# Kernel tuning notes

Measured on AMD Instinct MI355X. Metric: run time of the kernel, lower is better.

Reference implementation:

```python
import jax, jax.numpy as jnp
import numpy as np

D_MODEL = 1024
N_HEADS = 16
HEAD_DIM = D_MODEL // N_HEADS


def setup_inputs() -> dict:
    key = jax.random.key(0)
    k1, k2, k3 = jax.random.split(key, 3)
    B, T, C = 4, 2048, D_MODEL
    x = jax.random.normal(k1, (B, T, C), dtype=jnp.float32)
    # torch Linear weight is (out,in); store as (in,out) so y = x @ W
    w_qkv = jax.random.normal(k2, (C, 3 * C), dtype=jnp.float32) * (1.0 / np.sqrt(C))
    w_proj = jax.random.normal(k3, (C, C), dtype=jnp.float32) * (1.0 / np.sqrt(C))
    return {"x": x, "w_qkv": w_qkv, "w_proj": w_proj}


def reference(x, w_qkv, w_proj):
    B, T, C = x.shape
    H, Dh = N_HEADS, HEAD_DIM
    qkv = x @ w_qkv                        # (B,T,3C)
    q, k, v = jnp.split(qkv, 3, axis=-1)
    def heads(t):
        return t.reshape(B, T, H, Dh).transpose(0, 2, 1, 3)  # (B,H,T,Dh)
    q, k, v = heads(q), heads(k), heads(v)
    scores = jnp.einsum('bhqd,bhkd->bhqk', q, k) / np.sqrt(Dh).astype(np.float32)
    causal = jnp.tril(jnp.ones((T, T), dtype=bool))
    scores = jnp.where(causal, scores, -jnp.inf)
    attn = jax.nn.softmax(scores, axis=-1)
    y = jnp.einsum('bhqk,bhkd->bhqd', attn, v)  # (B,H,T,Dh)
    y = y.transpose(0, 2, 1, 3).reshape(B, T, C)
    return y @ w_proj
```

## Files before the change

### kernel.cpp

```cpp
#include <hip/hip_runtime.h>

#define SEQ_T 2048
#define NBATCH 4
#define CDIM 1024
#define NHEAD 16
#define MROWS 8192
#define QKVC 3072

typedef unsigned short u16;
typedef __bf16 bf16x8 __attribute__((ext_vector_type(8)));
typedef float f32x4 __attribute__((ext_vector_type(4)));
typedef unsigned short u16x8 __attribute__((ext_vector_type(8)));
typedef unsigned uint32x4 __attribute__((ext_vector_type(4)));

__device__ __forceinline__ u16 f32_to_bf16(float f) {
  union { float f; unsigned int u; } v; v.f = f;
  unsigned int u = v.u;
  unsigned int r = ((u >> 16) & 1u) + 0x7fffu;
  return (u16)((u + r) >> 16);
}

__device__ __forceinline__ void gload_lds16(const u16* g, u16* l) {
  __builtin_amdgcn_global_load_lds(
      (const __attribute__((address_space(1))) void*)g,
      (__attribute__((address_space(3))) void*)l, 16, 0, 0);
}

__global__ __launch_bounds__(256) void cast_bf16_kernel(const float* __restrict__ in,
                                                        u16* __restrict__ out, int n4) {
  int i = blockIdx.x * 256 + threadIdx.x;
  if (i >= n4) return;
  float4 v = ((const float4*)in)[i];
  ushort4 o;
  o.x = f32_to_bf16(v.x); o.y = f32_to_bf16(v.y);
  o.z = f32_to_bf16(v.z); o.w = f32_to_bf16(v.w);
  ((ushort4*)out)[i] = o;
}

__global__ void transpose_cast_kernel(const float* __restrict__ in, u16* __restrict__ out,
                                      int R, int Cc) {
  __shared__ float tile[32][33];
  int c0 = blockIdx.x * 32, r0 = blockIdx.y * 32;
  int tx = threadIdx.x, ty = threadIdx.y;
  #pragma unroll
  for (int i = 0; i < 32; i += 8)
    tile[ty + i][tx] = in[(size_t)(r0 + ty + i) * Cc + c0 + tx];
  __syncthreads();
  #pragma unroll
  for (int i = 0; i < 32; i += 8)
    out[(size_t)(c0 + ty + i) * R + r0 + tx] = f32_to_bf16(tile[tx][ty + i]);
}

__global__ __launch_bounds__(256) void repack_k_kernel(const u16* __restrict__ QKV,
                                                       u16* __restrict__ Kc) {
  const int kvt32 = blockIdx.x, bh = blockIdx.y;
  const int b = bh >> 4, h = bh & 15;
  const int tid = threadIdx.x;
  const int f = tid >> 6, l = tid & 63;
  const int t = f >> 1, i = f & 1;
  const int row = kvt32 * 32 + t * 16 + (l & 15);
  const bf16x8 v = *(const bf16x8*)(QKV + (size_t)b * SEQ_T * QKVC + (size_t)row * QKVC +
                                    CDIM + h * 64 + i * 32 + (l >> 4) * 8);
  *(bf16x8*)(Kc + (size_t)bh * 131072 + (size_t)kvt32 * 2048 + f * 512 + l * 8) = v;
}

__global__ void repack_v_kernel(const u16* __restrict__ QKV, u16* __restrict__ Vc) {
  __shared__ u16 tile[32][34];
  const int t0 = blockIdx.x * 32, d0 = blockIdx.y * 32;
  const int bh = blockIdx.z;
  const int b = bh >> 4, h = bh & 15;
  const int tx = threadIdx.x, ty = threadIdx.y;
  const u16* Vp = QKV + (size_t)b * SEQ_T * QKVC + 2 * CDIM + h * 64 + d0;
  #pragma unroll
  for (int i = 0; i < 32; i += 8)
    tile[ty + i][tx] = Vp[(size_t)(t0 + ty + i) * QKVC + tx];
  __syncthreads();
  const int tid = ty * 32 + tx;
  if (tid < 128) {
    const int bc = tid >> 2, ag = tid & 3;
    union { u16 u[8]; bf16x8 v; } o;
    #pragma unroll
    for (int j = 0; j < 8; ++j) o.u[j] = tile[ag * 8 + j][bc];
    const int dvl = d0 + bc;
    *(bf16x8*)(Vc + (size_t)bh * 131072 + (size_t)(t0 >> 5) * 2048 +
               (dvl >> 4) * 512 + ag * 128 + (dvl & 15) * 8) = o.v;
  }
}

template <typename OT, bool QSCALE>
__global__ __launch_bounds__(256, 3)
void gemm_bt_kernel(const u16* __restrict__ A, const u16* __restrict__ Bt,
                    OT* __restrict__ C, int N, int K) {
  __shared__ u16 sA[3][4096];
  __shared__ u16 sB[3][4096];
  const int tid = threadIdx.x;
  const int lane = tid & 63, w = tid >> 6;
  const int wm = w >> 1, wn = w & 1;
  const int l15 = lane & 15, lhi = lane >> 4;
  const int row0 = blockIdx.x * 128, col0 = blockIdx.y * 128;

  const int oln  = ((lane & 3) - (lane >> 2)) & 3;
  const int srow = w * 32 + (lane >> 2);
  const u16* aS = A  + (size_t)(row0 + srow) * K + oln * 8;
  const u16* bS = Bt + (size_t)(col0 + srow) * K + oln * 8;
  const int stD = w * 1024;
  const int rdA = (wm * 64 + l15) * 32 + ((lhi + l15) & 3) * 8;
  const int rdB = (wn * 64 + l15) * 32 + ((lhi + l15) & 3) * 8;

  f32x4 acc[4][4] = {};

#define STAGE(KT, S)                                                            \
  {                                                                             \
    const size_t ko = (size_t)(KT) * 32;                                        \
    gload_lds16(aS + ko,          &sA[S][stD]);                                 \
    gload_lds16(aS + ko + 16 * K, &sA[S][stD + 512]);                           \
    gload_lds16(bS + ko,          &sB[S][stD]);                                 \
    gload_lds16(bS + ko + 16 * K, &sB[S][stD + 512]);                           \
  }
#define COMPUTE(S)                                                              \
  {                                                                             \
    bf16x8 af[4], bf[4];                                                        \
    _Pragma("unroll") for (int mi = 0; mi < 4; ++mi)                            \
      af[mi] = *(const bf16x8*)&sA[S][rdA + mi * 512];                          \
    _Pragma("unroll") for (int ni = 0; ni < 4; ++ni)                            \
      bf[ni] = *(const bf16x8*)&sB[S][rdB + ni * 512];                          \
    __builtin_amdgcn_s_setprio(1);                                              \
    _Pragma("unroll") for (int mi = 0; mi < 4; ++mi)                            \
      _Pragma("unroll") for (int ni = 0; ni < 4; ++ni)                          \
        acc[mi][ni] = __builtin_amdgcn_mfma_f32_16x16x32_bf16(af[mi], bf[ni],   \
                                                              acc[mi][ni], 0, 0, 0); \
    __builtin_amdgcn_s_setprio(0);                                              \
  }
#define WAITBAR4                                                                \
  asm volatile("s_waitcnt vmcnt(4)" ::: "memory");                              \
  __builtin_amdgcn_sched_barrier(0);                                            \
  __builtin_amdgcn_s_barrier();

  STAGE(0, 0);
  STAGE(1, 1);
  WAITBAR4;

  #pragma unroll 1
  for (int kt = 0; kt < 30; kt += 3) {
    STAGE(kt + 2, 2); COMPUTE(0); WAITBAR4;
    STAGE(kt + 3, 0); COMPUTE(1); WAITBAR4;
    STAGE(kt + 4, 1); COMPUTE(2); WAITBAR4;
  }
  COMPUTE(0);
  asm volatile("s_waitcnt vmcnt(0)" ::: "memory");
  __builtin_amdgcn_sched_barrier(0);
  __builtin_amdgcn_s_barrier();
  COMPUTE(1);
#undef STAGE
#undef COMPUTE
#undef WAITBAR4

  #pragma unroll
  for (int mt = 0; mt < 4; ++mt)
    #pragma unroll
    for (int nt = 0; nt < 4; ++nt)
      #pragma unroll
      for (int r = 0; r < 4; ++r) {
        const int rr = row0 + wm * 64 + mt * 16 + lhi * 4 + r;
        const int cc = col0 + wn * 64 + nt * 16 + l15;
        float v = acc[mt][nt][r];
        if (QSCALE && cc < CDIM) v *= 0.18033688011f;
        if constexpr (sizeof(OT) == 2) C[(size_t)rr * N + cc] = f32_to_bf16(v);
        else                           C[(size_t)rr * N + cc] = v;
      }
}

template <bool DOMASK>
__device__ __forceinline__ void attn_step(const bf16x8 (&qf)[2],
                                          const bf16x8 (&kf)[2][2],
                                          const bf16x8 (&vb)[4],
                                          const bf16x8 ones,
                                          f32x4 (&acc)[4], f32x4& acc1,
                                          int l15, int lhi, int kv0, int qg) {
  f32x4 st[2];
  #pragma unroll
  for (int t = 0; t < 2; ++t) {
    f32x4 z = {0.f, 0.f, 0.f, 0.f};
    z = __builtin_amdgcn_mfma_f32_16x16x32_bf16(kf[t][0], qf[0], z, 0, 0, 0);
    z = __builtin_amdgcn_mfma_f32_16x16x32_bf16(kf[t][1], qf[1], z, 0, 0, 0);
    st[t] = z;
  }
  #pragma unroll
  for (int t = 0; t < 2; ++t)
    #pragma unroll
    for (int r = 0; r < 4; ++r) {
      float sv = st[t][r];
      if (DOMASK) {
        const int kvg = kv0 + t * 16 + lhi * 4 + r;
        sv = (kvg > qg) ? -__builtin_inff() : sv;
      }
      st[t][r] = exp2f(sv);
    }
  unsigned c00, c01, c10, c11;
  asm("v_cvt_pk_bf16_f32 %0, %1, %2" : "=v"(c00) : "v"(st[0][0]), "v"(st[0][1]));
  asm("v_cvt_pk_bf16_f32 %0, %1, %2" : "=v"(c01) : "v"(st[0][2]), "v"(st[0][3]));
  asm("v_cvt_pk_bf16_f32 %0, %1, %2" : "=v"(c10) : "v"(st[1][0]), "v"(st[1][1]));
  asm("v_cvt_pk_bf16_f32 %0, %1, %2" : "=v"(c11) : "v"(st[1][2]), "v"(st[1][3]));
  asm("v_permlane32_swap_b32 %0, %1" : "+v"(c00), "+v"(c10));
  asm("v_permlane32_swap_b32 %0, %1" : "+v"(c01), "+v"(c11));
  asm("v_permlane16_swap_b32 %0, %1" : "+v"(c00), "+v"(c10));
  asm("v_permlane16_swap_b32 %0, %1" : "+v"(c01), "+v"(c11));
  uint32x4 pw; pw[0] = c00; pw[1] = c01; pw[2] = c10; pw[3] = c11;
  const bf16x8 pa = __builtin_bit_cast(bf16x8, pw);
  #pragma unroll
  for (int d = 0; d < 4; ++d)
    acc[d] = __builtin_amdgcn_mfma_f32_16x16x32_bf16(pa, vb[d], acc[d], 0, 0, 0);
  acc1 = __builtin_amdgcn_mfma_f32_16x16x32_bf16(pa, ones, acc1, 0, 0, 0);
}

__global__ __launch_bounds__(256, 4) void attn_kernel(const u16* __restrict__ QKV,
                                                      const u16* __restrict__ Kc,
                                                      const u16* __restrict__ Vc,
                                                      u16* __restrict__ Y) {
  __shared__ u16 Kl[2][2048];
  __shared__ u16 Vl[2][2048];
  const int tid = threadIdx.x, lane = tid & 63, wid = tid >> 6;
  const int l15 = lane & 15, lhi = lane >> 4;
  const int id = blockIdx.x;
  const int xcd = id & 7, k = (id >> 3) & 15, hi3 = id >> 7;
  const int bh = hi3 * 8 + xcd;
  const int b = bh >> 4, h = bh & 15;
  const int pa = k * 4 + wid;
  const int qA0 = pa * 16, qB0 = (127 - pa) * 16;
  const int nchA = pa / 2 + 1, nchB = (127 - pa) / 2 + 1;
  const int ncmax = (127 - k * 4) / 2 + 1;
  const size_t base = (size_t)b * SEQ_T * QKVC;
  const u16* Qp  = QKV + base + h * 64;
  const u16* KcC = Kc + (size_t)bh * 131072;
  const u16* VcC = Vc + (size_t)bh * 131072;

  u16x8 ou;
  #pragma unroll
  for (int j = 0; j < 8; ++j) ou[j] = 0x3F80;
  const bf16x8 ones = __builtin_bit_cast(bf16x8, ou);

  gload_lds16(KcC + wid * 512 + lane * 8, &Kl[0][wid * 512]);
  gload_lds16(VcC + wid * 512 + lane * 8, &Vl[0][wid * 512]);

  bf16x8 qfA[2], qfB[2];
  #pragma unroll
  for (int i = 0; i < 2; ++i) {
    qfA[i] = *(const bf16x8*)(Qp + (size_t)(qA0 + l15) * QKVC + i * 32 + lhi * 8);
    qfB[i] = *(const bf16x8*)(Qp + (size_t)(qB0 + l15) * QKVC + i * 32 + lhi * 8);
  }
  const int qgA = qA0 + l15, qgB = qB0 + l15;

  f32x4 accA[4] = {}, accB[4] = {};
  f32x4 acc1A = {}, acc1B = {};

  __syncthreads();

  int cbuf = 0;
  for (int ic = 0; ic < ncmax; ++ic) {
    if (ic + 1 < ncmax) {
      const u16* kg = KcC + (size_t)(ic + 1) * 2048 + wid * 512 + lane * 8;
      const u16* vg = VcC + (size_t)(ic + 1) * 2048 + wid * 512 + lane * 8;
      gload_lds16(kg, &Kl[cbuf ^ 1][wid * 512]);
      gload_lds16(vg, &Vl[cbuf ^ 1][wid * 512]);
    }
    const u16* kb = &Kl[cbuf][0];
    const u16* vp = &Vl[cbuf][0];
    bf16x8 kf[2][2], vb[4];
    #pragma unroll
    for (int t = 0; t < 2; ++t)
      #pragma unroll
      for (int i = 0; i < 2; ++i)
        kf[t][i] = *(const bf16x8*)(kb + (t * 2 + i) * 512 + lane * 8);
    #pragma unroll
    for (int d = 0; d < 4; ++d)
      vb[d] = *(const bf16x8*)(vp + d * 512 + lane * 8);

    const int kv0 = ic * 32;
    if (ic < nchB) {
      if (ic == nchB - 1)
        attn_step<true>(qfB, kf, vb, ones, accB, acc1B, l15, lhi, kv0, qgB);
      else
        attn_step<false>(qfB, kf, vb, ones, accB, acc1B, l15, lhi, kv0, qgB);
    }
    if (ic < nchA) {
      if (ic == nchA - 1)
        attn_step<true>(qfA, kf, vb, ones, accA, acc1A, l15, lhi, kv0, qgA);
      else
        attn_step<false>(qfA, kf, vb, ones, accA, acc1A, l15, lhi, kv0, qgA);
    }
    __syncthreads();
    cbuf ^= 1;
  }

  u16* Yp = Y + (size_t)b * SEQ_T * CDIM + h * 64;
  #pragma unroll
  for (int r = 0; r < 4; ++r) {
    const float ivA = 1.0f / acc1A[r];
    const float ivB = 1.0f / acc1B[r];
    #pragma unroll
    for (int d = 0; d < 4; ++d) {
      Yp[(size_t)(qA0 + lhi * 4 + r) * CDIM + d * 16 + l15] = f32_to_bf16(accA[d][r] * ivA);
      Yp[(size_t)(qB0 + lhi * 4 + r) * CDIM + d * 16 + l15] = f32_to_bf16(accB[d][r] * ivB);
    }
  }
}

extern "C" void kernel_launch(void* const* d_in, const int* in_sizes, int n_in,
                              void* d_out, int out_size, void* d_ws, size_t ws_size,
                              hipStream_t stream) {
  const float* x      = (const float*)d_in[0];
  const float* w_qkv  = (const float*)d_in[1];
  const float* w_proj = (const float*)d_in[2];
  float* out = (float*)d_out;

  u16* Xb  = (u16*)d_ws;
  u16* Wqt = Xb  + (size_t)MROWS * CDIM;
  u16* Wpt = Wqt + (size_t)QKVC * CDIM;
  u16* QKV = Wpt + (size_t)CDIM * CDIM;
  u16* Yb  = QKV + (size_t)MROWS * QKVC;
  u16* Vc  = Yb  + (size_t)MROWS * CDIM;
  u16* Kc  = Xb;

  cast_bf16_kernel<<<(MROWS * CDIM / 4 + 255) / 256, 256, 0, stream>>>(x, Xb, MROWS * CDIM / 4);
  transpose_cast_kernel<<<dim3(QKVC / 32, CDIM / 32), dim3(32, 8), 0, stream>>>(w_qkv, Wqt, CDIM, QKVC);
  transpose_cast_kernel<<<dim3(CDIM / 32, CDIM / 32), dim3(32, 8), 0, stream>>>(w_proj, Wpt, CDIM, CDIM);

  gemm_bt_kernel<u16, true><<<dim3(MROWS / 128, QKVC / 128), 256, 0, stream>>>(Xb, Wqt, QKV, QKVC, CDIM);

  repack_k_kernel<<<dim3(SEQ_T / 32, NBATCH * NHEAD), 256, 0, stream>>>(QKV, Kc);
  repack_v_kernel<<<dim3(SEQ_T / 32, 2, NBATCH * NHEAD), dim3(32, 8), 0, stream>>>(QKV, Vc);

  attn_kernel<<<1024, 256, 0, stream>>>(QKV, Kc, Vc, Yb);

  gemm_bt_kernel<float, false><<<dim3(MROWS / 128, CDIM / 128), 256, 0, stream>>>(Yb, Wpt, out, CDIM, CDIM);
}
```

Baseline: 189.0 us.

## Pre-tile QKV GEMM operands into MFMA fragment layout and use 256x256 tiles

The cast kernels for x and w_qkv now write bf16 data directly in a 16x32 fragment-tiled layout, so each wave fetches a contiguous 1KB fragment. This lets the new GEMM load straight to LDS without swizzling. The QKV projection moves to a new 256x256-tile kernel with 512 threads, triple-buffered LDS and per-wave 128x64 accumulators, which raises arithmetic intensity. In exchange it uses more registers and LDS per block, and the grid shrinks to 384 blocks, which may underfill the 256 CUs.

After: 194.3 us. 2.8% more time.

```diff
diff --git a/kernel.cpp b/kernel.cpp
--- a/kernel.cpp
+++ b/kernel.cpp
@@ -26,15 +26,44 @@
       (__attribute__((address_space(3))) void*)l, 16, 0, 0);
 }
 
-__global__ __launch_bounds__(256) void cast_bf16_kernel(const float* __restrict__ in,
-                                                        u16* __restrict__ out, int n4) {
-  int i = blockIdx.x * 256 + threadIdx.x;
-  if (i >= n4) return;
-  float4 v = ((const float4*)in)[i];
-  ushort4 o;
-  o.x = f32_to_bf16(v.x); o.y = f32_to_bf16(v.y);
-  o.z = f32_to_bf16(v.z); o.w = f32_to_bf16(v.w);
-  ((ushort4*)out)[i] = o;
+
+__global__ __launch_bounds__(256) void cast_block_kernel(const float* __restrict__ in,
+                                                         u16* __restrict__ out) {
+  const int i = blockIdx.x * 256 + threadIdx.x;
+  const int kg = i & 127;
+  const int row = i >> 7;
+  const float4 v0 = ((const float4*)in)[i * 2];
+  const float4 v1 = ((const float4*)in)[i * 2 + 1];
+  union { u16 u[8]; bf16x8 b; } o;
+  o.u[0] = f32_to_bf16(v0.x); o.u[1] = f32_to_bf16(v0.y);
+  o.u[2] = f32_to_bf16(v0.z); o.u[3] = f32_to_bf16(v0.w);
+  o.u[4] = f32_to_bf16(v1.x); o.u[5] = f32_to_bf16(v1.y);
+  o.u[6] = f32_to_bf16(v1.z); o.u[7] = f32_to_bf16(v1.w);
+  const int tile = (row >> 4) * 32 + (kg >> 2);
+  const int lane = (row & 15) + ((kg & 3) << 4);
+  *(bf16x8*)(out + (size_t)tile * 512 + lane * 8) = o.b;
+}
+
+__global__ void transpose_cast_block_kernel(const float* __restrict__ in,
+                                            u16* __restrict__ out) {
+  __shared__ float tile[32][33];
+  const int c0 = blockIdx.x * 32, r0 = blockIdx.y * 32;
+  const int tx = threadIdx.x, ty = threadIdx.y;
+  #pragma unroll
+  for (int i = 0; i < 32; i += 8)
+    tile[ty + i][tx] = in[(size_t)(r0 + ty + i) * QKVC + c0 + tx];
+  __syncthreads();
+  const int t = ty * 32 + tx;
+  if (t < 128) {
+    const int cc = t & 31, kgq = t >> 5;
+    union { u16 u[8]; bf16x8 b; } o;
+    #pragma unroll
+    for (int j = 0; j < 8; ++j) o.u[j] = f32_to_bf16(tile[kgq * 8 + j][cc]);
+    const int rowN = c0 + cc;
+    const int tileI = (rowN >> 4) * 32 + (r0 >> 5);
+    const int lane = (rowN & 15) + (kgq << 4);
+    *(bf16x8*)(out + (size_t)tileI * 512 + lane * 8) = o.b;
+  }
 }
 
 __global__ void transpose_cast_kernel(const float* __restrict__ in, u16* __restrict__ out,
@@ -85,6 +114,84 @@
     *(bf16x8*)(Vc + (size_t)bh * 131072 + (size_t)(t0 >> 5) * 2048 +
                (dvl >> 4) * 512 + ag * 128 + (dvl & 15) * 8) = o.v;
   }
+}
+
+template <bool QSCALE>
+__global__ __launch_bounds__(512, 2)
+void gemm256_kernel(const u16* __restrict__ Ab, const u16* __restrict__ Bb,
+                    u16* __restrict__ C, int N) {
+  __shared__ u16 sA[3][8192];
+  __shared__ u16 sB[3][8192];
+  const int tid = threadIdx.x;
+  const int lane = tid & 63, w = tid >> 6;
+  const int wm = w >> 2, wn = w & 3;
+  const int l15 = lane & 15, lhi = lane >> 4;
+  const int row0 = blockIdx.x * 256, col0 = blockIdx.y * 256;
+
+  const u16* aT0 = Ab + ((size_t)((row0 >> 4) + w)     * 32) * 512 + lane * 8;
+  const u16* aT1 = Ab + ((size_t)((row0 >> 4) + 8 + w) * 32) * 512 + lane * 8;
+  const u16* bT0 = Bb + ((size_t)((col0 >> 4) + w)     * 32) * 512 + lane * 8;
+  const u16* bT1 = Bb + ((size_t)((col0 >> 4) + 8 + w) * 32) * 512 + lane * 8;
+
+  f32x4 acc[8][4] = {};
+
+#define STAGE(KT, S)                                                            \
+  {                                                                             \
+    gload_lds16(aT0 + (size_t)(KT) * 512, &sA[S][w * 512]);                     \
+    gload_lds16(aT1 + (size_t)(KT) * 512, &sA[S][(8 + w) * 512]);               \
+    gload_lds16(bT0 + (size_t)(KT) * 512, &sB[S][w * 512]);                     \
+    gload_lds16(bT1 + (size_t)(KT) * 512, &sB[S][(8 + w) * 512]);               \
+  }
+#define COMPUTE(S)                                                              \
+  {                                                                             \
+    bf16x8 bf[4];                                                               \
+    _Pragma("unroll") for (int ni = 0; ni < 4; ++ni)                            \
+      bf[ni] = *(const bf16x8*)&sB[S][(wn * 4 + ni) * 512 + lane * 8];          \
+    __builtin_amdgcn_s_setprio(1);                                              \
+    _Pragma("unroll") for (int mi = 0; mi < 8; ++mi) {                          \
+      const bf16x8 af = *(const bf16x8*)&sA[S][(wm * 8 + mi) * 512 + lane * 8]; \
+      _Pragma("unroll") for (int ni = 0; ni < 4; ++ni)                          \
+        acc[mi][ni] = __builtin_amdgcn_mfma_f32_16x16x32_bf16(af, bf[ni],       \
+                                                              acc[mi][ni], 0, 0, 0); \
+    }                                                                           \
+    __builtin_amdgcn_s_setprio(0);                                              \
+  }
+#define WAITBAR4                                                                \
+  asm volatile("s_waitcnt vmcnt(4)" ::: "memory");                              \
+  __builtin_amdgcn_sched_barrier(0);                                            \
+  __builtin_amdgcn_s_barrier();
+
+  STAGE(0, 0);
+  STAGE(1, 1);
+  WAITBAR4;
+
+  #pragma unroll 1
+  for (int kt = 0; kt < 30; kt += 3) {
+    STAGE(kt + 2, 2); COMPUTE(0); WAITBAR4;
+    STAGE(kt + 3, 0); COMPUTE(1); WAITBAR4;
+    STAGE(kt + 4, 1); COMPUTE(2); WAITBAR4;
+  }
+  COMPUTE(0);
+  asm volatile("s_waitcnt vmcnt(0)" ::: "memory");
+  __builtin_amdgcn_sched_barrier(0);
+  __builtin_amdgcn_s_barrier();
+  COMPUTE(1);
+#undef STAGE
+#undef COMPUTE
+#undef WAITBAR4
+
+  #pragma unroll
+  for (int mi = 0; mi < 8; ++mi)
+    #pragma unroll
+    for (int ni = 0; ni < 4; ++ni)
+      #pragma unroll
+      for (int r = 0; r < 4; ++r) {
+        const int rr = row0 + wm * 128 + mi * 16 + lhi * 4 + r;
+        const int cc = col0 + wn * 64 + ni * 16 + l15;
+        float v = acc[mi][ni][r];
+        if (QSCALE && cc < CDIM) v *= 0.18033688011f;
+        C[(size_t)rr * N + cc] = f32_to_bf16(v);
+      }
 }
 
 template <typename OT, bool QSCALE>
@@ -321,11 +428,11 @@
   u16* Vc  = Yb  + (size_t)MROWS * CDIM;
   u16* Kc  = Xb;
 
-  cast_bf16_kernel<<<(MROWS * CDIM / 4 + 255) / 256, 256, 0, stream>>>(x, Xb, MROWS * CDIM / 4);
-  transpose_cast_kernel<<<dim3(QKVC / 32, CDIM / 32), dim3(32, 8), 0, stream>>>(w_qkv, Wqt, CDIM, QKVC);
+  cast_block_kernel<<<MROWS * CDIM / 8 / 256, 256, 0, stream>>>(x, Xb);
+  transpose_cast_block_kernel<<<dim3(QKVC / 32, CDIM / 32), dim3(32, 8), 0, stream>>>(w_qkv, Wqt);
   transpose_cast_kernel<<<dim3(CDIM / 32, CDIM / 32), dim3(32, 8), 0, stream>>>(w_proj, Wpt, CDIM, CDIM);
 
-  gemm_bt_kernel<u16, true><<<dim3(MROWS / 128, QKVC / 128), 256, 0, stream>>>(Xb, Wqt, QKV, QKVC, CDIM);
+  gemm256_kernel<true><<<dim3(MROWS / 256, QKVC / 256), 512, 0, stream>>>(Xb, Wqt, QKV, QKVC);
 
   repack_k_kernel<<<dim3(SEQ_T / 32, NBATCH * NHEAD), 256, 0, stream>>>(QKV, Kc);
   repack_v_kernel<<<dim3(SEQ_T / 32, 2, NBATCH * NHEAD), dim3(32, 8), 0, stream>>>(QKV, Vc);
```

## Fuse K/V repacking into QKV GEMM epilogue and drop repack kernels

Applied to the files above, without the earlier changes.

The QKV projection GEMM epilogue now writes Q to a dense buffer and scatters K and V directly into the chunked layouts the attention kernel consumes. This removes the two repack kernels and the full QKV intermediate round-trip through memory. The cost is scattered 2-byte stores in the epilogue, which coalesce less well than the previous row-major writes. The workspace layout is changed to hold separate Q, K and V buffers.

New measurement: 183.3 us. 3.0% less time.

```diff
diff --git a/kernel.cpp b/kernel.cpp
--- a/kernel.cpp
+++ b/kernel.cpp
@@ -51,46 +51,11 @@
     out[(size_t)(c0 + ty + i) * R + r0 + tx] = f32_to_bf16(tile[tx][ty + i]);
 }
 
-__global__ __launch_bounds__(256) void repack_k_kernel(const u16* __restrict__ QKV,
-                                                       u16* __restrict__ Kc) {
-  const int kvt32 = blockIdx.x, bh = blockIdx.y;
-  const int b = bh >> 4, h = bh & 15;
-  const int tid = threadIdx.x;
-  const int f = tid >> 6, l = tid & 63;
-  const int t = f >> 1, i = f & 1;
-  const int row = kvt32 * 32 + t * 16 + (l & 15);
-  const bf16x8 v = *(const bf16x8*)(QKV + (size_t)b * SEQ_T * QKVC + (size_t)row * QKVC +
-                                    CDIM + h * 64 + i * 32 + (l >> 4) * 8);
-  *(bf16x8*)(Kc + (size_t)bh * 131072 + (size_t)kvt32 * 2048 + f * 512 + l * 8) = v;
-}
-
-__global__ void repack_v_kernel(const u16* __restrict__ QKV, u16* __restrict__ Vc) {
-  __shared__ u16 tile[32][34];
-  const int t0 = blockIdx.x * 32, d0 = blockIdx.y * 32;
-  const int bh = blockIdx.z;
-  const int b = bh >> 4, h = bh & 15;
-  const int tx = threadIdx.x, ty = threadIdx.y;
-  const u16* Vp = QKV + (size_t)b * SEQ_T * QKVC + 2 * CDIM + h * 64 + d0;
-  #pragma unroll
-  for (int i = 0; i < 32; i += 8)
-    tile[ty + i][tx] = Vp[(size_t)(t0 + ty + i) * QKVC + tx];
-  __syncthreads();
-  const int tid = ty * 32 + tx;
-  if (tid < 128) {
-    const int bc = tid >> 2, ag = tid & 3;
-    union { u16 u[8]; bf16x8 v; } o;
-    #pragma unroll
-    for (int j = 0; j < 8; ++j) o.u[j] = tile[ag * 8 + j][bc];
-    const int dvl = d0 + bc;
-    *(bf16x8*)(Vc + (size_t)bh * 131072 + (size_t)(t0 >> 5) * 2048 +
-               (dvl >> 4) * 512 + ag * 128 + (dvl & 15) * 8) = o.v;
-  }
-}
-
-template <typename OT, bool QSCALE>
+template <bool FUSE, typename OT>
 __global__ __launch_bounds__(256, 3)
 void gemm_bt_kernel(const u16* __restrict__ A, const u16* __restrict__ Bt,
-                    OT* __restrict__ C, int N, int K) {
+                    OT* __restrict__ C, u16* __restrict__ Kc, u16* __restrict__ Vc,
+                    int N, int K) {
   __shared__ u16 sA[3][4096];
   __shared__ u16 sB[3][4096];
   const int tid = threadIdx.x;
@@ -164,9 +129,28 @@
         const int rr = row0 + wm * 64 + mt * 16 + lhi * 4 + r;
         const int cc = col0 + wn * 64 + nt * 16 + l15;
         float v = acc[mt][nt][r];
-        if (QSCALE && cc < CDIM) v *= 0.18033688011f;
-        if constexpr (sizeof(OT) == 2) C[(size_t)rr * N + cc] = f32_to_bf16(v);
-        else                           C[(size_t)rr * N + cc] = v;
+        if constexpr (FUSE) {
+          if (cc < CDIM) {
+            ((u16*)C)[(size_t)rr * CDIM + cc] = f32_to_bf16(v * 0.18033688011f);
+          } else if (cc < 2 * CDIM) {
+            const int d = cc - CDIM;
+            const int h = d >> 6, dd = d & 63;
+            const int bb = rr >> 11, t = rr & 2047;
+            const size_t off = (size_t)(bb * 16 + h) * 131072 + (size_t)(t >> 5) * 2048
+                + (size_t)(((t >> 4) & 1) * 2 + (dd >> 5)) * 512
+                + ((dd >> 3) & 3) * 128 + (t & 15) * 8 + (dd & 7);
+            Kc[off] = f32_to_bf16(v);
+          } else {
+            const int d = cc - 2 * CDIM;
+            const int h = d >> 6, dv = d & 63;
+            const int bb = rr >> 11, t = rr & 2047;
+            const size_t off = (size_t)(bb * 16 + h) * 131072 + (size_t)(t >> 5) * 2048
+                + (size_t)(dv >> 4) * 512 + ((t >> 3) & 3) * 128 + (dv & 15) * 8 + (t & 7);
+            Vc[off] = f32_to_bf16(v);
+          }
+        } else {
+          C[(size_t)rr * N + cc] = v;
+        }
       }
 }
 
@@ -213,7 +197,7 @@
   acc1 = __builtin_amdgcn_mfma_f32_16x16x32_bf16(pa, ones, acc1, 0, 0, 0);
 }
 
-__global__ __launch_bounds__(256, 4) void attn_kernel(const u16* __restrict__ QKV,
+__global__ __launch_bounds__(256, 4) void attn_kernel(const u16* __restrict__ Qb,
                                                       const u16* __restrict__ Kc,
                                                       const u16* __restrict__ Vc,
                                                       u16* __restrict__ Y) {
@@ -229,8 +213,7 @@
   const int qA0 = pa * 16, qB0 = (127 - pa) * 16;
   const int nchA = pa / 2 + 1, nchB = (127 - pa) / 2 + 1;
   const int ncmax = (127 - k * 4) / 2 + 1;
-  const size_t base = (size_t)b * SEQ_T * QKVC;
-  const u16* Qp  = QKV + base + h * 64;
+  const u16* Qp  = Qb + (size_t)b * SEQ_T * CDIM + h * 64;
   const u16* KcC = Kc + (size_t)bh * 131072;
   const u16* VcC = Vc + (size_t)bh * 131072;
 
@@ -245,8 +228,8 @@
   bf16x8 qfA[2], qfB[2];
   #pragma unroll
   for (int i = 0; i < 2; ++i) {
-    qfA[i] = *(const bf16x8*)(Qp + (size_t)(qA0 + l15) * QKVC + i * 32 + lhi * 8);
-    qfB[i] = *(const bf16x8*)(Qp + (size_t)(qB0 + l15) * QKVC + i * 32 + lhi * 8);
+    qfA[i] = *(const bf16x8*)(Qp + (size_t)(qA0 + l15) * CDIM + i * 32 + lhi * 8);
+    qfB[i] = *(const bf16x8*)(Qp + (size_t)(qB0 + l15) * CDIM + i * 32 + lhi * 8);
   }
   const int qgA = qA0 + l15, qgB = qB0 + l15;
 
@@ -316,21 +299,20 @@
   u16* Xb  = (u16*)d_ws;
   u16* Wqt = Xb  + (size_t)MROWS * CDIM;
   u16* Wpt = Wqt + (size_t)QKVC * CDIM;
-  u16* QKV = Wpt + (size_t)CDIM * CDIM;
-  u16* Yb  = QKV + (size_t)MROWS * QKVC;
-  u16* Vc  = Yb  + (size_t)MROWS * CDIM;
-  u16* Kc  = Xb;
+  u16* Qb  = Wpt + (size_t)CDIM * CDIM;
+  u16* Kc  = Qb  + (size_t)MROWS * CDIM;
+  u16* Vc  = Kc  + (size_t)64 * 131072;
+  u16* Yb  = Vc  + (size_t)64 * 131072;
 
   cast_bf16_kernel<<<(MROWS * CDIM / 4 + 255) / 256, 256, 0, stream>>>(x, Xb, MROWS * CDIM / 4);
   transpose_cast_kernel<<<dim3(QKVC / 32, CDIM / 32), dim3(32, 8), 0, stream>>>(w_qkv, Wqt, CDIM, QKVC);
   transpose_cast_kernel<<<dim3(CDIM / 32, CDIM / 32), dim3(32, 8), 0, stream>>>(w_proj, Wpt, CDIM, CDIM);
 
-  gemm_bt_kernel<u16, true><<<dim3(MROWS / 128, QKVC / 128), 256, 0, stream>>>(Xb, Wqt, QKV, QKVC, CDIM);
-
-  repack_k_kernel<<<dim3(SEQ_T / 32, NBATCH * NHEAD), 256, 0, stream>>>(QKV, Kc);
-  repack_v_kernel<<<dim3(SEQ_T / 32, 2, NBATCH * NHEAD), dim3(32, 8), 0, stream>>>(QKV, Vc);
-
-  attn_kernel<<<1024, 256, 0, stream>>>(QKV, Kc, Vc, Yb);
-
-  gemm_bt_kernel<float, false><<<dim3(MROWS / 128, CDIM / 128), 256, 0, stream>>>(Yb, Wpt, out, CDIM, CDIM);
-}
+  gemm_bt_kernel<true, u16><<<dim3(MROWS / 128, QKVC / 128), 256, 0, stream>>>(
+      Xb, Wqt, Qb, Kc, Vc, QKVC, CDIM);
+
+  attn_kernel<<<1024, 256, 0, stream>>>(Qb, Kc, Vc, Yb);
+
+  gemm_bt_kernel<false, float><<<dim3(MROWS / 128, CDIM / 128), 256, 0, stream>>>(
+      Yb, Wpt, out, nullptr, nullptr, CDIM, CDIM);
+}
```
